# Performance work log

Measured on AMD Instinct MI355X. Metric: run time of the kernel, lower is better.

## Reference

```python
import jax, jax.numpy as jnp
import numpy as np

B = 4194304  # batch of affine parameter vectors


def setup_inputs() -> dict:
    key = jax.random.key(0)
    vector = jax.random.normal(key, (B, 6), dtype=jnp.float32)
    return {"vector": vector}


def reference(vector):
    # vector: [B, 6] = (tx, ty, tz, angle_x, angle_y, angle_z)
    t = vector[:, :3]                      # [B, 3] translation
    ax, ay, az = vector[:, 3], vector[:, 4], vector[:, 5]

    cx, sx = jnp.cos(ax), jnp.sin(ax)
    cy, sy = jnp.cos(ay), jnp.sin(ay)
    cz, sz = jnp.cos(az), jnp.sin(az)
    one = jnp.ones_like(cx)
    zero = jnp.zeros_like(cx)

    # Batched 3x3 rotation matrices, rows stacked then columns: [B, 3, 3]
    x_rot = jnp.stack([
        jnp.stack([one, zero, zero], -1),
        jnp.stack([zero, cx, -sx], -1),
        jnp.stack([zero, sx, cx], -1),
    ], axis=-2)
    y_rot = jnp.stack([
        jnp.stack([cy, zero, sy], -1),
        jnp.stack([zero, one, zero], -1),
        jnp.stack([-sy, zero, cy], -1),
    ], axis=-2)
    z_rot = jnp.stack([
        jnp.stack([cz, -sz, zero], -1),
        jnp.stack([sz, cz, zero], -1),
        jnp.stack([zero, zero, one], -1),
    ], axis=-2)

    m_rot = jnp.einsum('bij,bjk,bkl->bil', x_rot, y_rot, z_rot)
    m_rot = m_rot - jnp.eye(3, dtype=vector.dtype)  # subtract identity (voxelmorph shift convention)

    matrix = jnp.concatenate([m_rot, t[:, :, None]], axis=2)  # [B, 3, 4]
    return matrix.reshape(vector.shape[0], 12)
```

## Files before the change

### kernel.cpp

```cpp
#include <hip/hip_runtime.h>


#define BLOCK 256
#define RPB   512

__device__ __forceinline__ int swz(int i) { return i ^ ((i >> 3) & 7); }

__global__ __launch_bounds__(BLOCK) void affine_to_matrix_staged(
    const float* __restrict__ in, float* __restrict__ out) {
    __shared__ float s_in[RPB * 6];
    __shared__ float s_out[RPB * 12];

    const int tid = threadIdx.x;
    const size_t rowBase = (size_t)blockIdx.x * RPB;
    const float4* gin  = reinterpret_cast<const float4*>(in  + rowBase * 6);
    float4*       gout = reinterpret_cast<float4*>(out + rowBase * 12);

    float4* s_in4 = reinterpret_cast<float4*>(s_in);
    #pragma unroll
    for (int k = 0; k < 3; ++k) {
        int g = tid + k * BLOCK;
        s_in4[g] = gin[g];
    }
    __syncthreads();

    const float4* myin = reinterpret_cast<const float4*>(s_in + tid * 12);
    float4 a = myin[0], b = myin[1], c = myin[2];
    float r[12] = {a.x, a.y, a.z, a.w, b.x, b.y, b.z, b.w, c.x, c.y, c.z, c.w};
    float4* s_out4 = reinterpret_cast<float4*>(s_out);
    #pragma unroll
    for (int k2 = 0; k2 < 2; ++k2) {
        const float* v = r + k2 * 6;
        float sx, cx, sy, cy, sz, cz;
        __sincosf(v[3], &sx, &cx);
        __sincosf(v[4], &sy, &cy);
        __sincosf(v[5], &sz, &cz);
        float sxsy = sx * sy;
        float cxsy = cx * sy;
        int base = tid * 6 + k2 * 3;
        s_out4[swz(base + 0)] = make_float4(cy * cz - 1.0f,      -cy * sz,                    sy,             v[0]);
        s_out4[swz(base + 1)] = make_float4(cx * sz + sxsy * cz, cx * cz - sxsy * sz - 1.0f,  -sx * cy,       v[1]);
        s_out4[swz(base + 2)] = make_float4(sx * sz - cxsy * cz, sx * cz + cxsy * sz,         cx * cy - 1.0f, v[2]);
    }
    __syncthreads();

    #pragma unroll
    for (int k = 0; k < 6; ++k) {
        int g = tid + k * BLOCK;
        gout[g] = s_out4[swz(g)];
    }
}

__global__ __launch_bounds__(BLOCK) void affine_to_matrix_tail(
    const float* __restrict__ in, float* __restrict__ out,
    size_t rowStart, size_t nRows) {
    size_t i = rowStart + blockIdx.x * (size_t)BLOCK + threadIdx.x;
    if (i >= nRows) return;
    const float* v = in + i * 6;
    float sx, cx, sy, cy, sz, cz;
    __sincosf(v[3], &sx, &cx);
    __sincosf(v[4], &sy, &cy);
    __sincosf(v[5], &sz, &cz);
    float sxsy = sx * sy, cxsy = cx * sy;
    float* m = out + i * 12;
    m[0] = cy * cz - 1.0f;      m[1] = -cy * sz;                   m[2]  = sy;              m[3]  = v[0];
    m[4] = cx * sz + sxsy * cz; m[5] = cx * cz - sxsy * sz - 1.0f; m[6]  = -sx * cy;        m[7]  = v[1];
    m[8] = sx * sz - cxsy * cz; m[9] = sx * cz + cxsy * sz;        m[10] = cx * cy - 1.0f;  m[11] = v[2];
}

extern "C" void kernel_launch(void* const* d_in, const int* in_sizes, int n_in,
                              void* d_out, int out_size, void* d_ws, size_t ws_size,
                              hipStream_t stream) {
    const float* in = (const float*)d_in[0];
    float* out = (float*)d_out;
    size_t rows = (size_t)in_sizes[0] / 6;
    size_t fullBlocks = rows / RPB;
    if (fullBlocks) {
        affine_to_matrix_staged<<<(unsigned)fullBlocks, BLOCK, 0, stream>>>(in, out);
    }
    size_t rem = rows - fullBlocks * RPB;
    if (rem) {
        unsigned tailGrid = (unsigned)((rem + BLOCK - 1) / BLOCK);
        affine_to_matrix_tail<<<tailGrid, BLOCK, 0, stream>>>(in, out, fullBlocks * RPB, rows);
    }
}
```

Before: 50.86 us.

## Process one row per thread with 256-row blocks instead of two

Halves rows per block so each thread computes a single affine matrix instead of two. Input staging shrinks to 1.5 float4 per thread, read back as float2 pairs, and output write-out drops to 3 float4 per thread. This doubles the grid size and cuts shared memory and registers per block, aiming for better occupancy and latency hiding. The cost is more blocks, more per-block overhead, and less work per thread to amortize the barriers.

```diff
diff --git a/kernel.cpp b/kernel.cpp
--- a/kernel.cpp
+++ b/kernel.cpp
@@ -2,7 +2,7 @@
 
 
 #define BLOCK 256
-#define RPB   512
+#define RPB   256
 
 __device__ __forceinline__ int swz(int i) { return i ^ ((i >> 3) & 7); }
 
@@ -17,35 +17,33 @@
     float4*       gout = reinterpret_cast<float4*>(out + rowBase * 12);
 
     float4* s_in4 = reinterpret_cast<float4*>(s_in);
-    #pragma unroll
-    for (int k = 0; k < 3; ++k) {
-        int g = tid + k * BLOCK;
-        s_in4[g] = gin[g];
+    {
+        s_in4[tid] = gin[tid];
+        int g = tid + BLOCK;
+        if (g < RPB * 6 / 4) s_in4[g] = gin[g];
     }
     __syncthreads();
 
-    const float4* myin = reinterpret_cast<const float4*>(s_in + tid * 12);
-    float4 a = myin[0], b = myin[1], c = myin[2];
-    float r[12] = {a.x, a.y, a.z, a.w, b.x, b.y, b.z, b.w, c.x, c.y, c.z, c.w};
+    const float2* myin = reinterpret_cast<const float2*>(s_in + tid * 6);
+    float2 a = myin[0], b = myin[1], c = myin[2];
+    float tx = a.x, ty = a.y, tz = b.x;
+    float ax = b.y, ay = c.x, az = c.y;
+
+    float sx, cx, sy, cy, sz, cz;
+    __sincosf(ax, &sx, &cx);
+    __sincosf(ay, &sy, &cy);
+    __sincosf(az, &sz, &cz);
+    float sxsy = sx * sy;
+    float cxsy = cx * sy;
     float4* s_out4 = reinterpret_cast<float4*>(s_out);
-    #pragma unroll
-    for (int k2 = 0; k2 < 2; ++k2) {
-        const float* v = r + k2 * 6;
-        float sx, cx, sy, cy, sz, cz;
-        __sincosf(v[3], &sx, &cx);
-        __sincosf(v[4], &sy, &cy);
-        __sincosf(v[5], &sz, &cz);
-        float sxsy = sx * sy;
-        float cxsy = cx * sy;
-        int base = tid * 6 + k2 * 3;
-        s_out4[swz(base + 0)] = make_float4(cy * cz - 1.0f,      -cy * sz,                    sy,             v[0]);
-        s_out4[swz(base + 1)] = make_float4(cx * sz + sxsy * cz, cx * cz - sxsy * sz - 1.0f,  -sx * cy,       v[1]);
-        s_out4[swz(base + 2)] = make_float4(sx * sz - cxsy * cz, sx * cz + cxsy * sz,         cx * cy - 1.0f, v[2]);
-    }
+    int base = tid * 3;
+    s_out4[swz(base + 0)] = make_float4(cy * cz - 1.0f,      -cy * sz,                    sy,             tx);
+    s_out4[swz(base + 1)] = make_float4(cx * sz + sxsy * cz, cx * cz - sxsy * sz - 1.0f,  -sx * cy,       ty);
+    s_out4[swz(base + 2)] = make_float4(sx * sz - cxsy * cz, sx * cz + cxsy * sz,         cx * cy - 1.0f, tz);
     __syncthreads();
 
     #pragma unroll
-    for (int k = 0; k < 6; ++k) {
+    for (int k = 0; k < 3; ++k) {
         int g = tid + k * BLOCK;
         gout[g] = s_out4[swz(g)];
     }
```

New measurement: 52.61 us. 3.5% more time.
